# Optimization experiments

Measured on AMD Instinct MI355X. Metric: run time of the kernel, lower is better.

The kernel has to match this reference:

```python
import jax, jax.numpy as jnp
import numpy as np

EPS = 1e-6

def setup_inputs() -> dict:
    key = jax.random.key(0)
    k = jax.random.split(key, 5)
    G, in_g, out_g = 16, 64, 64
    x = jax.random.normal(k[0], (G * in_g, 8, 64, 64), dtype=jnp.float32)
    ln_gamma = 1.0 + 0.1 * jax.random.normal(k[1], (G, in_g), dtype=jnp.float32)
    ln_beta = 0.1 * jax.random.normal(k[2], (G, in_g), dtype=jnp.float32)
    W = jax.random.normal(k[3], (G, out_g, in_g), dtype=jnp.float32) / np.sqrt(in_g)
    b = 0.1 * jax.random.normal(k[4], (G, out_g), dtype=jnp.float32)
    return {"x": x, "ln_gamma": ln_gamma, "ln_beta": ln_beta, "W": W, "b": b}


def reference(x, ln_gamma, ln_beta, W, b):
    # x: [C_in, D1, D2, D3]; W: [G, out_g, in_g]; faithful to torch reshape semantics
    G, out_g, in_g = W.shape
    D1, D2, D3 = x.shape[1:]
    xg = x.reshape(G, D1, D2, D3, in_g)            # row-major reshape, same as torch
    # per-group LayerNorm over last dim (biased variance, eps=1e-6)
    mu = jnp.mean(xg, axis=-1, keepdims=True)
    var = jnp.mean(jnp.square(xg - mu), axis=-1, keepdims=True)
    xn = (xg - mu) * jax.lax.rsqrt(var + EPS)
    xn = xn * ln_gamma[:, None, None, None, :] + ln_beta[:, None, None, None, :]
    # per-group Linear: y_g = xn_g @ W_g^T + b_g  -> [G, D1, D2, D3, out_g]
    y = jnp.einsum('gabck,gok->gabco', xn, W) + b[:, None, None, None, :]
    # torch.cat(list_of_groups, dim=-1): groups become the fastest-varying blocks of last dim
    y = jnp.moveaxis(y, 0, -2).reshape(D1, D2, D3, G * out_g)
    # permute([3, 0, 1, 2]) -> [C_out, D1, D2, D3]
    return jnp.transpose(y, (3, 0, 1, 2))
```

## Files before the change

kernel.cpp:

```cpp
#include <hip/hip_runtime.h>

typedef __attribute__((ext_vector_type(4))) float f32x4;
typedef __attribute__((ext_vector_type(8))) short bf16x8;

__device__ __forceinline__ short bf16_rne(float f) {
    unsigned int u = __float_as_uint(f);
    u += 0x7FFFu + ((u >> 16) & 1u);
    return (short)(u >> 16);
}


__global__ __launch_bounds__(256, 2)
void gln_mfma_kernel(const float* __restrict__ x,
                     const float* __restrict__ gamma,
                     const float* __restrict__ beta,
                     const float* __restrict__ W,
                     const float* __restrict__ bias,
                     float* __restrict__ out)
{
    const int tid  = threadIdx.x;
    const int lane = tid & 63;
    const int w    = blockIdx.x * 4 + (tid >> 6);
    const int g    = w >> 9;
    const int rr0  = (w & 511) << 6;

    const int l15 = lane & 15;
    const int l4  = lane >> 4;
    const int ks  = l4 * 8;

    bf16x8 bfrag[4][2];
    {
        const float* Wg = W + (size_t)(g * 64) * 64;
        #pragma unroll
        for (int ot = 0; ot < 4; ++ot) {
            const float* wrow = Wg + (size_t)(ot * 16 + l15) * 64;
            #pragma unroll
            for (int kc = 0; kc < 2; ++kc) {
                f32x4 w0 = *(const f32x4*)(wrow + kc * 32 + ks);
                f32x4 w1 = *(const f32x4*)(wrow + kc * 32 + ks + 4);
                bf16x8 f;
                #pragma unroll
                for (int j = 0; j < 4; ++j) { f[j] = bf16_rne(w0[j]); f[j + 4] = bf16_rne(w1[j]); }
                bfrag[ot][kc] = f;
            }
        }
    }

    float gk[16], bk[16];
    {
        const float* gp = gamma + g * 64;
        const float* bp = beta  + g * 64;
        #pragma unroll
        for (int kc = 0; kc < 2; ++kc) {
            f32x4 g0 = *(const f32x4*)(gp + kc * 32 + ks);
            f32x4 g1 = *(const f32x4*)(gp + kc * 32 + ks + 4);
            f32x4 b0 = *(const f32x4*)(bp + kc * 32 + ks);
            f32x4 b1 = *(const f32x4*)(bp + kc * 32 + ks + 4);
            #pragma unroll
            for (int j = 0; j < 4; ++j) {
                gk[kc * 8 + j] = g0[j]; gk[kc * 8 + 4 + j] = g1[j];
                bk[kc * 8 + j] = b0[j]; bk[kc * 8 + 4 + j] = b1[j];
            }
        }
    }

    float bo[4];
    #pragma unroll
    for (int ot = 0; ot < 4; ++ot) bo[ot] = bias[g * 64 + ot * 16 + l15];

    const float* xg = x   + (size_t)g * 32768 * 64;
    float* outg     = out + (size_t)g * 64 * 32768;

    f32x4 buf[2][4];
    {
        const float* rowp = xg + (size_t)(rr0 + l15) * 64;
        buf[0][0] = *(const f32x4*)(rowp + ks);
        buf[0][1] = *(const f32x4*)(rowp + ks + 4);
        buf[0][2] = *(const f32x4*)(rowp + 32 + ks);
        buf[0][3] = *(const f32x4*)(rowp + 32 + ks + 4);
    }

    f32x4 vout[4][4];

    #pragma unroll
    for (int t = 0; t < 4; ++t) {
        if (t + 1 < 4) {
            const float* rowp = xg + (size_t)(rr0 + (t + 1) * 16 + l15) * 64;
            buf[(t + 1) & 1][0] = *(const f32x4*)(rowp + ks);
            buf[(t + 1) & 1][1] = *(const f32x4*)(rowp + ks + 4);
            buf[(t + 1) & 1][2] = *(const f32x4*)(rowp + 32 + ks);
            buf[(t + 1) & 1][3] = *(const f32x4*)(rowp + 32 + ks + 4);
        }

        float s = 0.f, s2 = 0.f;
        #pragma unroll
        for (int i = 0; i < 4; ++i) {
            #pragma unroll
            for (int j = 0; j < 4; ++j) {
                float v = buf[t & 1][i][j];
                s += v; s2 += v * v;
            }
        }
        s  += __shfl_xor(s, 16, 64);  s  += __shfl_xor(s, 32, 64);
        s2 += __shfl_xor(s2, 16, 64); s2 += __shfl_xor(s2, 32, 64);
        const float mu   = s * (1.0f / 64.0f);
        const float var  = s2 * (1.0f / 64.0f) - mu * mu;
        const float rstd = rsqrtf(var + 1e-6f);

        bf16x8 a0, a1;
        #pragma unroll
        for (int j = 0; j < 8; ++j) {
            float c1 = rstd * gk[j];
            float v  = buf[t & 1][j >> 2][j & 3] * c1 + (bk[j] - mu * c1);
            a0[j] = bf16_rne(v);
        }
        #pragma unroll
        for (int j = 0; j < 8; ++j) {
            float c1 = rstd * gk[8 + j];
            float v  = buf[t & 1][2 + (j >> 2)][j & 3] * c1 + (bk[8 + j] - mu * c1);
            a1[j] = bf16_rne(v);
        }

        #pragma unroll
        for (int ot = 0; ot < 4; ++ot) {
            f32x4 acc = {0.f, 0.f, 0.f, 0.f};
            acc = __builtin_amdgcn_mfma_f32_16x16x32_bf16(a0, bfrag[ot][0], acc, 0, 0, 0);
            acc = __builtin_amdgcn_mfma_f32_16x16x32_bf16(a1, bfrag[ot][1], acc, 0, 0, 0);
            #pragma unroll
            for (int q = 0; q < 4; ++q) acc[q] += bo[ot];
            vout[t][ot] = acc;
        }
    }

    #pragma unroll
    for (int ot = 0; ot < 4; ++ot) {
        float* base = outg + (size_t)(ot * 16 + l15) * 32768 + rr0 + l4 * 4;
        #pragma unroll
        for (int t = 0; t < 4; ++t) {
            float* dst = base + t * 16;
            asm volatile("global_store_dwordx4 %0, %1, off sc0 sc1 nt"
                         :: "v"(dst), "v"(vout[t][ot]) : "memory");
        }
    }
}

extern "C" void kernel_launch(void* const* d_in, const int* in_sizes, int n_in,
                              void* d_out, int out_size, void* d_ws, size_t ws_size,
                              hipStream_t stream) {
    const float* x     = (const float*)d_in[0];
    const float* gamma = (const float*)d_in[1];
    const float* beta  = (const float*)d_in[2];
    const float* W     = (const float*)d_in[3];
    const float* b     = (const float*)d_in[4];
    float* out = (float*)d_out;

    dim3 grid(2048), block(256);
    hipLaunchKernelGGL(gln_mfma_kernel, grid, block, 0, stream, x, gamma, beta, W, b, out);
}
```

Measured before the change: 53.18 us.

## Stage x tiles through LDS with async global_load_lds triple buffering

Replaces per-lane register double-buffered global loads of x with direct global-to-LDS async loads (global_load_lds), using three LDS stages per wave and an XOR swizzle to avoid bank conflicts. Three tiles are issued up front, before the W/gamma loads, so more memory traffic is in flight; the fourth tile reuses stage 0 after it is read. Manual vmcnt waits order the stages. This costs 48KB of LDS per block, which may limit occupancy, and adds LDS read latency.

```diff
diff --git a/kernel.cpp b/kernel.cpp
--- a/kernel.cpp
+++ b/kernel.cpp
@@ -2,6 +2,9 @@
 
 typedef __attribute__((ext_vector_type(4))) float f32x4;
 typedef __attribute__((ext_vector_type(8))) short bf16x8;
+
+typedef const __attribute__((address_space(1))) float* gas1p;
+typedef __attribute__((address_space(3))) float* las3p;
 
 __device__ __forceinline__ short bf16_rne(float f) {
     unsigned int u = __float_as_uint(f);
@@ -18,15 +21,39 @@
                      const float* __restrict__ bias,
                      float* __restrict__ out)
 {
+    __shared__ __align__(16) float xlds[4][3][1024];
+
     const int tid  = threadIdx.x;
     const int lane = tid & 63;
-    const int w    = blockIdx.x * 4 + (tid >> 6);
+    const int wv   = tid >> 6;
+    const int w    = blockIdx.x * 4 + wv;
     const int g    = w >> 9;
     const int rr0  = (w & 511) << 6;
 
     const int l15 = lane & 15;
     const int l4  = lane >> 4;
     const int ks  = l4 * 8;
+
+    const float* xg = x   + (size_t)g * 32768 * 64;
+    float* outg     = out + (size_t)g * 64 * 32768;
+
+    auto issue_tile = [&](int t, int s) {
+        const float* tb = xg + (size_t)(rr0 + t * 16) * 64;
+        #pragma unroll
+        for (int j = 0; j < 4; ++j) {
+            const int p   = j * 64 + lane;
+            const int row = p >> 4;
+            const int cl  = p & 15;
+            const float* src = tb + row * 64 + ((cl ^ (row & 7)) << 2);
+            __builtin_amdgcn_global_load_lds((gas1p)src,
+                (las3p)(&xlds[wv][s][j * 256]), 16, 0, 0);
+        }
+    };
+
+    issue_tile(0, 0);
+    issue_tile(1, 1);
+    issue_tile(2, 2);
+    __builtin_amdgcn_sched_barrier(0);
 
     bf16x8 bfrag[4][2];
     {
@@ -68,38 +95,33 @@
     #pragma unroll
     for (int ot = 0; ot < 4; ++ot) bo[ot] = bias[g * 64 + ot * 16 + l15];
 
-    const float* xg = x   + (size_t)g * 32768 * 64;
-    float* outg     = out + (size_t)g * 64 * 32768;
-
-    f32x4 buf[2][4];
-    {
-        const float* rowp = xg + (size_t)(rr0 + l15) * 64;
-        buf[0][0] = *(const f32x4*)(rowp + ks);
-        buf[0][1] = *(const f32x4*)(rowp + ks + 4);
-        buf[0][2] = *(const f32x4*)(rowp + 32 + ks);
-        buf[0][3] = *(const f32x4*)(rowp + 32 + ks + 4);
-    }
-
     f32x4 vout[4][4];
+    const int swz = l15 & 7;
 
     #pragma unroll
     for (int t = 0; t < 4; ++t) {
-        if (t + 1 < 4) {
-            const float* rowp = xg + (size_t)(rr0 + (t + 1) * 16 + l15) * 64;
-            buf[(t + 1) & 1][0] = *(const f32x4*)(rowp + ks);
-            buf[(t + 1) & 1][1] = *(const f32x4*)(rowp + ks + 4);
-            buf[(t + 1) & 1][2] = *(const f32x4*)(rowp + 32 + ks);
-            buf[(t + 1) & 1][3] = *(const f32x4*)(rowp + 32 + ks + 4);
+        if (t == 3)      asm volatile("s_waitcnt vmcnt(0)" ::: "memory");
+        else if (t == 2) asm volatile("s_waitcnt vmcnt(4)" ::: "memory");
+        else             asm volatile("s_waitcnt vmcnt(8)" ::: "memory");
+        __builtin_amdgcn_sched_barrier(0);
+
+        const float* sp = &xlds[wv][t % 3][0];
+        f32x4 v0 = *(const f32x4*)(sp + l15 * 64 + (((2 * l4)     ^ swz) << 2));
+        f32x4 v1 = *(const f32x4*)(sp + l15 * 64 + (((2 * l4 + 1) ^ swz) << 2));
+        f32x4 v2 = *(const f32x4*)(sp + l15 * 64 + (((8 + 2 * l4) ^ swz) << 2));
+        f32x4 v3 = *(const f32x4*)(sp + l15 * 64 + (((9 + 2 * l4) ^ swz) << 2));
+
+        if (t == 0) {
+            asm volatile("s_waitcnt lgkmcnt(0)" ::: "memory");
+            __builtin_amdgcn_sched_barrier(0);
+            issue_tile(3, 0);
         }
 
         float s = 0.f, s2 = 0.f;
         #pragma unroll
-        for (int i = 0; i < 4; ++i) {
-            #pragma unroll
-            for (int j = 0; j < 4; ++j) {
-                float v = buf[t & 1][i][j];
-                s += v; s2 += v * v;
-            }
+        for (int j = 0; j < 4; ++j) {
+            s += v0[j] + v1[j] + v2[j] + v3[j];
+            s2 += v0[j]*v0[j] + v1[j]*v1[j] + v2[j]*v2[j] + v3[j]*v3[j];
         }
         s  += __shfl_xor(s, 16, 64);  s  += __shfl_xor(s, 32, 64);
         s2 += __shfl_xor(s2, 16, 64); s2 += __shfl_xor(s2, 32, 64);
@@ -109,16 +131,15 @@
 
         bf16x8 a0, a1;
         #pragma unroll
-        for (int j = 0; j < 8; ++j) {
+        for (int j = 0; j < 4; ++j) {
             float c1 = rstd * gk[j];
-            float v  = buf[t & 1][j >> 2][j & 3] * c1 + (bk[j] - mu * c1);
-            a0[j] = bf16_rne(v);
-        }
-        #pragma unroll
-        for (int j = 0; j < 8; ++j) {
-            float c1 = rstd * gk[8 + j];
-            float v  = buf[t & 1][2 + (j >> 2)][j & 3] * c1 + (bk[8 + j] - mu * c1);
-            a1[j] = bf16_rne(v);
+            a0[j]     = bf16_rne(v0[j] * c1 + (bk[j] - mu * c1));
+            float c2 = rstd * gk[4 + j];
+            a0[4 + j] = bf16_rne(v1[j] * c2 + (bk[4 + j] - mu * c2));
+            float c3 = rstd * gk[8 + j];
+            a1[j]     = bf16_rne(v2[j] * c3 + (bk[8 + j] - mu * c3));
+            float c4 = rstd * gk[12 + j];
+            a1[4 + j] = bf16_rne(v3[j] * c4 + (bk[12 + j] - mu * c4));
         }
 
         #pragma unroll
```

New measurement: 49.38 us (median of 2 runs). -7.1%, faster.
